# Performance work log

Hardware: AMD Instinct MI355X
Metric: run time of the kernel (lower is better)

## Reference

```python
import jax, jax.numpy as jnp
import numpy as np

D_MODEL = 1024
D_FF = 4096
NUM_EXPERTS = 8
TOP_K = 2


def setup_inputs() -> dict:
    key = jax.random.key(0)
    ks = jax.random.split(key, 8)
    s_in = 1.0 / np.sqrt(D_MODEL)
    s_ff = 1.0 / np.sqrt(D_FF)
    x = jax.random.normal(ks[0], (2, 2048, D_MODEL), dtype=jnp.float32)
    Wg = jax.random.uniform(ks[1], (D_MODEL, NUM_EXPERTS), minval=-s_in, maxval=s_in, dtype=jnp.float32)
    bg = jax.random.uniform(ks[2], (NUM_EXPERTS,), minval=-s_in, maxval=s_in, dtype=jnp.float32)
    W1 = jax.random.uniform(ks[3], (NUM_EXPERTS, D_MODEL, D_FF), minval=-s_in, maxval=s_in, dtype=jnp.float32)
    b1 = jax.random.uniform(ks[4], (NUM_EXPERTS, D_FF), minval=-s_in, maxval=s_in, dtype=jnp.float32)
    W2 = jax.random.uniform(ks[5], (NUM_EXPERTS, D_FF, D_MODEL), minval=-s_ff, maxval=s_ff, dtype=jnp.float32)
    b2 = jax.random.uniform(ks[6], (NUM_EXPERTS, D_MODEL), minval=-s_ff, maxval=s_ff, dtype=jnp.float32)
    return {"x": x, "Wg": Wg, "bg": bg, "W1": W1, "b1": b1, "W2": W2, "b2": b2}


def reference(x, Wg, bg, W1, b1, W2, b2):
    # Gating: softmax over experts, top-k, renormalize
    gate_logits = jnp.einsum('bsd,de->bse', x, Wg) + bg
    gate_probs = jax.nn.softmax(gate_logits, axis=-1)
    topk_probs, topk_idx = jax.lax.top_k(gate_probs, TOP_K)
    topk_probs = topk_probs / jnp.sum(topk_probs, axis=-1, keepdims=True)
    # Per-token combine weights over experts [B,S,E] (top-k indices are unique)
    onehot = jax.nn.one_hot(topk_idx, NUM_EXPERTS, dtype=x.dtype)  # [B,S,K,E]
    weights = jnp.einsum('bske,bsk->bse', onehot, topk_probs)
    # Dense per-expert FFN (exact GELU matches torch nn.GELU default)
    h = jnp.einsum('bsd,edf->bsef', x, W1) + b1  # [B,S,E,Dff]
    h = jax.nn.gelu(h, approximate=False)
    y = jnp.einsum('bsef,efd->bsed', h, W2) + b2  # [B,S,E,D]
    return jnp.einsum('bsed,bse->bsd', y, weights)
```

## Files before the change

kernel.cpp:

```cpp
#include <hip/hip_runtime.h>
#include <hip/hip_bf16.h>
#include <math.h>

#define D_MODEL 1024
#define D_FF    4096
#define NE      8
#define NTOK    4096
#define MAXTOK  4096
#define MAXROWS 9216
#define MAXMT   72

typedef __attribute__((ext_vector_type(8))) short short8;
typedef __attribute__((ext_vector_type(4))) float f32x4;

#define WS_CNT     0
#define WS_OFFA    128
#define WS_TOKIDS  1024
#define WS_TOKW    (WS_TOKIDS + NE*MAXTOK*4)
#define WS_ROWTOK  (WS_TOKW + NE*MAXTOK*4)
#define WS_ROWW    (WS_ROWTOK + MAXROWS*4)
#define WS_XG      524288
#define WS_H       (WS_XG + (size_t)MAXROWS*D_MODEL*2)
#define WS_W1T     (WS_H + (size_t)MAXROWS*D_FF*2)
#define WS_W2T     (WS_W1T + (size_t)NE*D_MODEL*D_FF*2)
#define WS_NEED    (WS_W2T + (size_t)NE*D_MODEL*D_FF*2)

__device__ __forceinline__ ushort f2b(float v) {
    __hip_bfloat16 b = __float2bfloat16(v);
    return *reinterpret_cast<ushort*>(&b);
}

__device__ __forceinline__ float gelu_f(float v) {
    float z = fabsf(v) * 0.70710678118654752f;
    float t = 1.0f / (1.0f + 0.3275911f * z);
    float p = t * (0.254829592f + t * (-0.284496736f + t * (1.421413741f + t * (-1.453152027f + t * 1.061405429f))));
    float er = 1.0f - p * __expf(-z * z);
    float s = (v >= 0.0f) ? er : -er;
    return 0.5f * v * (1.0f + s);
}

__device__ __forceinline__ int xcd_swz(int orig, int nwg) {
    int q = nwg >> 3, r = nwg & 7;
    int xcd = orig & 7, pos = orig >> 3;
    return (xcd < r ? xcd * (q + 1) : r * (q + 1) + (xcd - r) * q) + pos;
}

__global__ __launch_bounds__(256) void gating_kernel(
    const float* __restrict__ x, const float* __restrict__ Wg, const float* __restrict__ bg,
    int* __restrict__ cnt, int* __restrict__ tok_ids, float* __restrict__ tok_w)
{
    __shared__ float s_wg[D_MODEL * NE];
    int tid = threadIdx.x;
    for (int i = tid; i < D_MODEL * NE; i += 256) s_wg[i] = Wg[i];
    __syncthreads();

    int t = blockIdx.x * 256 + tid;
    float acc[NE];
    #pragma unroll
    for (int e = 0; e < NE; ++e) acc[e] = bg[e];
    const float* xr = x + (size_t)t * D_MODEL;
    for (int d = 0; d < D_MODEL; d += 4) {
        float4 xv = *reinterpret_cast<const float4*>(xr + d);
        #pragma unroll
        for (int e = 0; e < NE; ++e) {
            acc[e] += xv.x * s_wg[(d + 0) * NE + e];
            acc[e] += xv.y * s_wg[(d + 1) * NE + e];
            acc[e] += xv.z * s_wg[(d + 2) * NE + e];
            acc[e] += xv.w * s_wg[(d + 3) * NE + e];
        }
    }
    int i0 = 0;
    #pragma unroll
    for (int e = 1; e < NE; ++e) if (acc[e] > acc[i0]) i0 = e;
    int i1 = (i0 == 0) ? 1 : 0;
    #pragma unroll
    for (int e = 0; e < NE; ++e) if (e != i0 && acc[e] > acc[i1]) i1 = e;
    float e1 = __expf(acc[i1] - acc[i0]);
    float inv = 1.0f / (1.0f + e1);
    float w0 = inv, w1 = e1 * inv;

    int p0 = atomicAdd(&cnt[i0], 1);
    tok_ids[i0 * MAXTOK + p0] = t;  tok_w[i0 * MAXTOK + p0] = w0;
    int p1 = atomicAdd(&cnt[i1], 1);
    tok_ids[i1 * MAXTOK + p1] = t;  tok_w[i1 * MAXTOK + p1] = w1;
}

__global__ void scan_kernel(const int* __restrict__ cnt, int* __restrict__ off) {
    if (threadIdx.x == 0) {
        int acc = 0;
        for (int e = 0; e < NE; ++e) { off[e] = acc; acc += ((cnt[e] + 127) & ~127); }
        off[NE] = acc;
    }
}

__global__ __launch_bounds__(256) void gather_kernel(
    const float* __restrict__ x, const int* __restrict__ cnt, const int* __restrict__ off,
    const int* __restrict__ tok_ids, const float* __restrict__ tok_w,
    ushort* __restrict__ Xg, int* __restrict__ rowtok, float* __restrict__ roww)
{
    int e = blockIdx.y;
    int npad = off[e + 1] - off[e];
    int r0 = blockIdx.x * 128;
    if (r0 >= npad) return;
    int n = cnt[e];
    int base = off[e];
    for (int idx = threadIdx.x; idx < 128 * 128; idx += 256) {
        int r = r0 + (idx >> 7);
        int s = idx & 127;
        int R = base + r;
        int tok = -1;
        float4 v0 = {0, 0, 0, 0}, v1 = {0, 0, 0, 0};
        if (r < n) {
            tok = tok_ids[e * MAXTOK + r];
            const float4* src = (const float4*)(x + (size_t)tok * D_MODEL + s * 8);
            v0 = src[0]; v1 = src[1];
        }
        ushort o[8];
        o[0] = f2b(v0.x); o[1] = f2b(v0.y); o[2] = f2b(v0.z); o[3] = f2b(v0.w);
        o[4] = f2b(v1.x); o[5] = f2b(v1.y); o[6] = f2b(v1.z); o[7] = f2b(v1.w);
        int c = s >> 3, sub = s & 7;
        int ds = sub ^ (R & 7);
        *(uint4*)(Xg + (size_t)R * D_MODEL + c * 64 + ds * 8) = *(const uint4*)o;
        if (s == 0) {
            rowtok[R] = tok;
            roww[R] = (tok >= 0) ? tok_w[e * MAXTOK + r] : 0.0f;
        }
    }
}

__global__ __launch_bounds__(256) void wconv_kernel(
    const float* __restrict__ src, ushort* __restrict__ dst, int K, int N)
{
    __shared__ float st[64][65];
    int e = blockIdx.z;
    int n0 = blockIdx.x * 64;
    int k0 = blockIdx.y * 64;
    const float* s = src + (size_t)e * K * N;
    ushort* d = dst + (size_t)e * N * K;
    for (int i = threadIdx.x; i < 4096; i += 256) {
        int kr = i >> 6, nc = i & 63;
        st[kr][nc] = s[(size_t)(k0 + kr) * N + n0 + nc];
    }
    __syncthreads();
    int c = k0 >> 6;
    #pragma unroll
    for (int it = 0; it < 2; ++it) {
        int v = threadIdx.x + it * 256;
        int nl = v >> 3, sub = v & 7;
        ushort o[8];
        #pragma unroll
        for (int j = 0; j < 8; ++j) o[j] = f2b(st[sub * 8 + j][nl]);
        int ds = sub ^ (nl & 7);
        *(uint4*)(d + (size_t)(n0 + nl) * K + c * 64 + ds * 8) = *(const uint4*)o;
    }
}

__global__ __launch_bounds__(256) void gemm1_kernel(
    const ushort* __restrict__ Xg, const ushort* __restrict__ W1T,
    const float* __restrict__ b1, const int* __restrict__ off,
    ushort* __restrict__ H)
{
    __shared__ ushort sA[2][128 * 64];
    __shared__ ushort sB[2][128 * 64];
    int wid = xcd_swz(blockIdx.x, MAXMT * 32);
    int mt = wid >> 5;
    int nt = wid & 31;
    int row0 = mt << 7;
    if (row0 >= off[NE]) return;
    int e = 0;
    #pragma unroll
    for (int i = 1; i < NE; ++i) if (off[i] <= row0) e = i;
    int nb0 = nt << 7;

    int tid = threadIdx.x;
    int lane = tid & 63, wave = tid >> 6;
    int wr = wave >> 1, wc = wave & 1;
    int lrow = tid >> 3, lslot = tid & 7;

    const ushort* Abase = Xg + (size_t)row0 * D_MODEL;
    const ushort* Bbase = W1T + ((size_t)e * D_FF + nb0) * D_MODEL;

    f32x4 acc[4][4];
    #pragma unroll
    for (int m = 0; m < 4; ++m)
        #pragma unroll
        for (int n = 0; n < 4; ++n)
            acc[m][n] = (f32x4){0.f, 0.f, 0.f, 0.f};

    #define STAGE1(buf, kt) { \
        _Pragma("unroll") \
        for (int r = 0; r < 4; ++r) { \
            int row = r * 32 + lrow; \
            const ushort* ga = Abase + (size_t)row * D_MODEL + (kt) * 64 + lslot * 8; \
            const ushort* gb = Bbase + (size_t)row * D_MODEL + (kt) * 64 + lslot * 8; \
            __builtin_amdgcn_global_load_lds((const __attribute__((address_space(1))) void*)ga, \
                (__attribute__((address_space(3))) void*)(sA[buf] + (size_t)(r * 256 + wave * 64) * 8), 16, 0, 0); \
            __builtin_amdgcn_global_load_lds((const __attribute__((address_space(1))) void*)gb, \
                (__attribute__((address_space(3))) void*)(sB[buf] + (size_t)(r * 256 + wave * 64) * 8), 16, 0, 0); \
        } }

    STAGE1(0, 0);
    __syncthreads();
    for (int kt = 0; kt < D_MODEL / 64; ++kt) {
        int cur = kt & 1;
        if (kt + 1 < D_MODEL / 64) STAGE1(cur ^ 1, kt + 1);
        #pragma unroll
        for (int ks = 0; ks < 2; ++ks) {
            short8 a[4], b[4];
            #pragma unroll
            for (int m = 0; m < 4; ++m) {
                int arow = wr * 64 + m * 16 + (lane & 15);
                int aslot = (ks * 4 + (lane >> 4)) ^ (arow & 7);
                a[m] = *(const short8*)(sA[cur] + arow * 64 + aslot * 8);
            }
            #pragma unroll
            for (int n = 0; n < 4; ++n) {
                int brow = wc * 64 + n * 16 + (lane & 15);
                int bslot = (ks * 4 + (lane >> 4)) ^ (brow & 7);
                b[n] = *(const short8*)(sB[cur] + brow * 64 + bslot * 8);
            }
            #pragma unroll
            for (int m = 0; m < 4; ++m)
                #pragma unroll
                for (int n = 0; n < 4; ++n)
                    acc[m][n] = __builtin_amdgcn_mfma_f32_16x16x32_bf16(a[m], b[n], acc[m][n], 0, 0, 0);
        }
        __syncthreads();
    }

    const float* b1e = b1 + (size_t)e * D_FF;
    #pragma unroll
    for (int m = 0; m < 4; ++m) {
        int rbase = wr * 64 + m * 16 + (lane >> 4) * 4;
        #pragma unroll
        for (int n = 0; n < 4; ++n) {
            int col = nb0 + wc * 64 + n * 16 + (lane & 15);
            float bv = b1e[col];
            int cc = col >> 6, sub = (col >> 3) & 7, el = col & 7;
            #pragma unroll
            for (int q = 0; q < 4; ++q) {
                int R = row0 + rbase + q;
                float v = gelu_f(acc[m][n][q] + bv);
                int ds = sub ^ (R & 7);
                H[(size_t)R * D_FF + cc * 64 + ds * 8 + el] = f2b(v);
            }
        }
    }
}

__global__ __launch_bounds__(256) void gemm2_kernel(
    const ushort* __restrict__ H, const ushort* __restrict__ W2T,
    const float* __restrict__ b2, const int* __restrict__ off,
    const int* __restrict__ rowtok, const float* __restrict__ roww,
    float* __restrict__ out)
{
    __shared__ ushort sA[2][128 * 64];
    __shared__ ushort sB[2][128 * 64];
    int wid = xcd_swz(blockIdx.x, MAXMT * 16);
    int mt = wid >> 4;
    int ks2 = (wid >> 3) & 1;
    int nt = wid & 7;
    int row0 = mt << 7;
    if (row0 >= off[NE]) return;
    int e = 0;
    #pragma unroll
    for (int i = 1; i < NE; ++i) if (off[i] <= row0) e = i;
    int nb0 = nt << 7;

    int tid = threadIdx.x;
    int lane = tid & 63, wave = tid >> 6;
    int wr = wave >> 1, wc = wave & 1;
    int lrow = tid >> 3, lslot = tid & 7;

    const ushort* Abase = H + (size_t)row0 * D_FF;
    const ushort* Bbase = W2T + ((size_t)e * D_MODEL + nb0) * D_FF;

    f32x4 acc[4][4];
    #pragma unroll
    for (int m = 0; m < 4; ++m)
        #pragma unroll
        for (int n = 0; n < 4; ++n)
            acc[m][n] = (f32x4){0.f, 0.f, 0.f, 0.f};

    #define STAGE2(buf, kt) { \
        _Pragma("unroll") \
        for (int r = 0; r < 4; ++r) { \
            int row = r * 32 + lrow; \
            const ushort* ga = Abase + (size_t)row * D_FF + (kt) * 64 + lslot * 8; \
            const ushort* gb = Bbase + (size_t)row * D_FF + (kt) * 64 + lslot * 8; \
            __builtin_amdgcn_global_load_lds((const __attribute__((address_space(1))) void*)ga, \
                (__attribute__((address_space(3))) void*)(sA[buf] + (size_t)(r * 256 + wave * 64) * 8), 16, 0, 0); \
            __builtin_amdgcn_global_load_lds((const __attribute__((address_space(1))) void*)gb, \
                (__attribute__((address_space(3))) void*)(sB[buf] + (size_t)(r * 256 + wave * 64) * 8), 16, 0, 0); \
        } }

    int kt0 = ks2 * 32;
    STAGE2(0, kt0);
    __syncthreads();
    for (int i = 0; i < 32; ++i) {
        int cur = i & 1;
        if (i + 1 < 32) STAGE2(cur ^ 1, kt0 + i + 1);
        #pragma unroll
        for (int ks = 0; ks < 2; ++ks) {
            short8 a[4], b[4];
            #pragma unroll
            for (int m = 0; m < 4; ++m) {
                int arow = wr * 64 + m * 16 + (lane & 15);
                int aslot = (ks * 4 + (lane >> 4)) ^ (arow & 7);
                a[m] = *(const short8*)(sA[cur] + arow * 64 + aslot * 8);
            }
            #pragma unroll
            for (int n = 0; n < 4; ++n) {
                int brow = wc * 64 + n * 16 + (lane & 15);
                int bslot = (ks * 4 + (lane >> 4)) ^ (brow & 7);
                b[n] = *(const short8*)(sB[cur] + brow * 64 + bslot * 8);
            }
            #pragma unroll
            for (int m = 0; m < 4; ++m)
                #pragma unroll
                for (int n = 0; n < 4; ++n)
                    acc[m][n] = __builtin_amdgcn_mfma_f32_16x16x32_bf16(a[m], b[n], acc[m][n], 0, 0, 0);
        }
        __syncthreads();
    }

    const float* b2e = b2 + (size_t)e * D_MODEL;
    #pragma unroll
    for (int m = 0; m < 4; ++m) {
        int rbase = wr * 64 + m * 16 + (lane >> 4) * 4;
        #pragma unroll
        for (int n = 0; n < 4; ++n) {
            int col = nb0 + wc * 64 + n * 16 + (lane & 15);
            float bv = (ks2 == 0) ? b2e[col] : 0.0f;
            #pragma unroll
            for (int q = 0; q < 4; ++q) {
                int R = row0 + rbase + q;
                int tok = rowtok[R];
                if (tok >= 0) {
                    float y = roww[R] * (acc[m][n][q] + bv);
                    atomicAdd(out + (size_t)tok * D_MODEL + col, y);
                }
            }
        }
    }
}

#define TM      32
#define FFC     128
#define KSTEP   64

__global__ __launch_bounds__(512) void ffn_kernel(
    const float* __restrict__ x,
    const float* __restrict__ W1, const float* __restrict__ b1,
    const float* __restrict__ W2, const float* __restrict__ b2,
    const int* __restrict__ cnt, const int* __restrict__ tok_ids, const float* __restrict__ tok_w,
    float* __restrict__ out)
{
    int e = blockIdx.y;
    int n = cnt[e];
    int t0 = blockIdx.x * TM;
    if (t0 >= n) return;
    int tid = threadIdx.x;

    __shared__ int   s_tok[TM];
    __shared__ float s_w[TM];
    __shared__ float s_x[TM][KSTEP];
    __shared__ float s_w1[KSTEP][FFC];
    __shared__ float s_h[TM][FFC];

    if (tid < TM) {
        int idx = t0 + tid;
        s_tok[tid] = (idx < n) ? tok_ids[e * MAXTOK + idx] : -1;
        s_w[tid]   = (idx < n) ? tok_w[e * MAXTOK + idx] : 0.0f;
    }
    __syncthreads();

    float acc[TM][2];
    #pragma unroll
    for (int i = 0; i < TM; ++i) { acc[i][0] = 0.0f; acc[i][1] = 0.0f; }

    const float* W1e = W1 + (size_t)e * D_MODEL * D_FF;
    const float* W2e = W2 + (size_t)e * D_FF * D_MODEL;
    const float* b1e = b1 + (size_t)e * D_FF;

    int ffl = (tid & 63) * 2;
    int g   = tid >> 6;

    int fb0 = blockIdx.z * (D_FF / 2);
    for (int fb = fb0; fb < fb0 + D_FF / 2; fb += FFC) {
        float bv0 = b1e[fb + ffl], bv1 = b1e[fb + ffl + 1];
        float hacc[4][2];
        #pragma unroll
        for (int j = 0; j < 4; ++j) { hacc[j][0] = bv0; hacc[j][1] = bv1; }

        for (int kb = 0; kb < D_MODEL; kb += KSTEP) {
            #pragma unroll
            for (int r = 0; r < 4; ++r) {
                int i = tid + 512 * r;
                int row = i >> 6, col = i & 63;
                int tok = s_tok[row];
                s_x[row][col] = (tok >= 0) ? x[(size_t)tok * D_MODEL + kb + col] : 0.0f;
            }
            #pragma unroll
            for (int r = 0; r < 16; ++r) {
                int i = tid + 512 * r;
                int row = i >> 7, col = i & 127;
                s_w1[row][col] = W1e[(size_t)(kb + row) * D_FF + fb + col];
            }
            __syncthreads();
            #pragma unroll 8
            for (int kk = 0; kk < KSTEP; ++kk) {
                float2 wv = *reinterpret_cast<const float2*>(&s_w1[kk][ffl]);
                #pragma unroll
                for (int j = 0; j < 4; ++j) {
                    float xv = s_x[g * 4 + j][kk];
                    hacc[j][0] += xv * wv.x;
                    hacc[j][1] += xv * wv.y;
                }
            }
            __syncthreads();
        }
        #pragma unroll
        for (int j = 0; j < 4; ++j) {
            #pragma unroll
            for (int p = 0; p < 2; ++p) {
                float v = hacc[j][p];
                v = 0.5f * v * (1.0f + erff(v * 0.70710678118654752f));
                s_h[g * 4 + j][ffl + p] = v;
            }
        }
        __syncthreads();
        for (int ff = 0; ff < FFC; ++ff) {
            const float* w2row = W2e + (size_t)(fb + ff) * D_MODEL;
            float wc0 = w2row[tid], wc1 = w2row[tid + 512];
            #pragma unroll
            for (int tt = 0; tt < TM; ++tt) {
                float hv = s_h[tt][ff];
                acc[tt][0] += hv * wc0;
                acc[tt][1] += hv * wc1;
            }
        }
        __syncthreads();
    }

    float bc0 = b2[(size_t)e * D_MODEL + tid];
    float bc1 = b2[(size_t)e * D_MODEL + tid + 512];
    if (blockIdx.z != 0) { bc0 = 0.0f; bc1 = 0.0f; }
    #pragma unroll
    for (int tt = 0; tt < TM; ++tt) {
        int tok = s_tok[tt];
        if (tok >= 0) {
            float w = s_w[tt];
            atomicAdd(&out[(size_t)tok * D_MODEL + tid],       w * (acc[tt][0] + bc0));
            atomicAdd(&out[(size_t)tok * D_MODEL + tid + 512], w * (acc[tt][1] + bc1));
        }
    }
}

extern "C" void kernel_launch(void* const* d_in, const int* in_sizes, int n_in,
                              void* d_out, int out_size, void* d_ws, size_t ws_size,
                              hipStream_t stream) {
    const float* x  = (const float*)d_in[0];
    const float* Wg = (const float*)d_in[1];
    const float* bg = (const float*)d_in[2];
    const float* W1 = (const float*)d_in[3];
    const float* b1 = (const float*)d_in[4];
    const float* W2 = (const float*)d_in[5];
    const float* b2 = (const float*)d_in[6];
    float* out = (float*)d_out;

    char* ws = (char*)d_ws;
    int*    cnt     = (int*)(ws + WS_CNT);
    int*    offp    = (int*)(ws + WS_OFFA);
    int*    tok_ids = (int*)(ws + WS_TOKIDS);
    float*  tok_w   = (float*)(ws + WS_TOKW);

    hipMemsetAsync(cnt, 0, NE * sizeof(int), stream);
    hipMemsetAsync(out, 0, (size_t)out_size * sizeof(float), stream);

    gating_kernel<<<NTOK / 256, 256, 0, stream>>>(x, Wg, bg, cnt, tok_ids, tok_w);

    if (ws_size >= WS_NEED) {
        int*    rowtok = (int*)(ws + WS_ROWTOK);
        float*  roww   = (float*)(ws + WS_ROWW);
        ushort* Xg     = (ushort*)(ws + WS_XG);
        ushort* Hb     = (ushort*)(ws + WS_H);
        ushort* W1T    = (ushort*)(ws + WS_W1T);
        ushort* W2T    = (ushort*)(ws + WS_W2T);

        scan_kernel<<<1, 64, 0, stream>>>(cnt, offp);
        wconv_kernel<<<dim3(D_FF / 64, D_MODEL / 64, NE), 256, 0, stream>>>(W1, W1T, D_MODEL, D_FF);
        wconv_kernel<<<dim3(D_MODEL / 64, D_FF / 64, NE), 256, 0, stream>>>(W2, W2T, D_FF, D_MODEL);
        gather_kernel<<<dim3(32, NE), 256, 0, stream>>>(x, cnt, offp, tok_ids, tok_w, Xg, rowtok, roww);
        gemm1_kernel<<<MAXMT * 32, 256, 0, stream>>>(Xg, W1T, b1, offp, Hb);
        gemm2_kernel<<<MAXMT * 16, 256, 0, stream>>>(Hb, W2T, b2, offp, rowtok, roww, out);
    } else {
        dim3 grid(MAXTOK / TM, NE, 2);
        ffn_kernel<<<grid, 512, 0, stream>>>(x, W1, b1, W2, b2, cnt, tok_ids, tok_w, out);
    }
}
```

Measured before the change: 570.3 us.

## Use 256x256 GEMM tiles with split-K partial buffers and deterministic combine kernel

Adds a new path that pads expert segments to 256 rows and runs both expert GEMMs with 256x256 tiles on 512-thread blocks, raising arithmetic intensity per LDS load. GEMM2 now writes split-K partial outputs into a workspace buffer (aliasing the dead W1T region) instead of atomically accumulating into the output. A per-token combine kernel sums the partials and applies gate weights, which removes the output memset and the atomics. The cost is more padding rows, an extra kernel with extra fp32 traffic, and a larger workspace requirement, with the old 128-tile path kept as a fallback.

After: 482.1 us. -15.5%, faster.

```diff
diff --git a/kernel.cpp b/kernel.cpp
--- a/kernel.cpp
+++ b/kernel.cpp
@@ -7,8 +7,11 @@
 #define NE      8
 #define NTOK    4096
 #define MAXTOK  4096
-#define MAXROWS 9216
-#define MAXMT   72
+
+#define MAXROWS 10240
+#define MAXMT   40
+#define MAXROWSB 9216
+#define MAXMTB   72
 
 typedef __attribute__((ext_vector_type(8))) short short8;
 typedef __attribute__((ext_vector_type(4))) float f32x4;
@@ -19,11 +22,19 @@
 #define WS_TOKW    (WS_TOKIDS + NE*MAXTOK*4)
 #define WS_ROWTOK  (WS_TOKW + NE*MAXTOK*4)
 #define WS_ROWW    (WS_ROWTOK + MAXROWS*4)
-#define WS_XG      524288
-#define WS_H       (WS_XG + (size_t)MAXROWS*D_MODEL*2)
-#define WS_W1T     (WS_H + (size_t)MAXROWS*D_FF*2)
-#define WS_W2T     (WS_W1T + (size_t)NE*D_MODEL*D_FF*2)
-#define WS_NEED    (WS_W2T + (size_t)NE*D_MODEL*D_FF*2)
+#define WS_TOKEXP  (WS_ROWW + MAXROWS*4)
+
+#define WS_H       524288
+#define WS_W1T     (WS_H   + (size_t)MAXROWS*D_FF*2)
+#define WS_XG      (WS_W1T + (size_t)NE*D_MODEL*D_FF*2)
+#define WS_W2T     (WS_XG  + (size_t)MAXROWS*D_MODEL*2)
+#define WS_NEED_A  (WS_W2T + (size_t)NE*D_MODEL*D_FF*2)
+
+#define WSB_XG     524288
+#define WSB_H      (WSB_XG  + (size_t)MAXROWSB*D_MODEL*2)
+#define WSB_W1T    (WSB_H   + (size_t)MAXROWSB*D_FF*2)
+#define WSB_W2T    (WSB_W1T + (size_t)NE*D_MODEL*D_FF*2)
+#define WS_NEED_B  (WSB_W2T + (size_t)NE*D_MODEL*D_FF*2)
 
 __device__ __forceinline__ ushort f2b(float v) {
     __hip_bfloat16 b = __float2bfloat16(v);
@@ -47,7 +58,8 @@
 
 __global__ __launch_bounds__(256) void gating_kernel(
     const float* __restrict__ x, const float* __restrict__ Wg, const float* __restrict__ bg,
-    int* __restrict__ cnt, int* __restrict__ tok_ids, float* __restrict__ tok_w)
+    int* __restrict__ cnt, int* __restrict__ tok_ids, float* __restrict__ tok_w,
+    int* __restrict__ tokexp)
 {
     __shared__ float s_wg[D_MODEL * NE];
     int tid = threadIdx.x;
@@ -81,11 +93,20 @@
 
     int p0 = atomicAdd(&cnt[i0], 1);
     tok_ids[i0 * MAXTOK + p0] = t;  tok_w[i0 * MAXTOK + p0] = w0;
+    tokexp[t * 2 + 0] = i0 * MAXTOK + p0;
     int p1 = atomicAdd(&cnt[i1], 1);
     tok_ids[i1 * MAXTOK + p1] = t;  tok_w[i1 * MAXTOK + p1] = w1;
-}
-
-__global__ void scan_kernel(const int* __restrict__ cnt, int* __restrict__ off) {
+    tokexp[t * 2 + 1] = i1 * MAXTOK + p1;
+}
+
+__global__ void scan256_kernel(const int* __restrict__ cnt, int* __restrict__ off) {
+    if (threadIdx.x == 0) {
+        int acc = 0;
+        for (int e = 0; e < NE; ++e) { off[e] = acc; acc += ((cnt[e] + 255) & ~255); }
+        off[NE] = acc;
+    }
+}
+__global__ void scan128_kernel(const int* __restrict__ cnt, int* __restrict__ off) {
     if (threadIdx.x == 0) {
         int acc = 0;
         for (int e = 0; e < NE; ++e) { off[e] = acc; acc += ((cnt[e] + 127) & ~127); }
@@ -155,14 +176,224 @@
     }
 }
 
-__global__ __launch_bounds__(256) void gemm1_kernel(
+
+__global__ __launch_bounds__(512, 2) void gemm1_256(
     const ushort* __restrict__ Xg, const ushort* __restrict__ W1T,
     const float* __restrict__ b1, const int* __restrict__ off,
     ushort* __restrict__ H)
 {
+    __shared__ ushort smem[65536];
+    int wid = xcd_swz(blockIdx.x, MAXMT * 16);
+    int mt = wid >> 4, nt = wid & 15;
+    int row0 = mt << 8;
+    if (row0 >= off[NE]) return;
+    int e = 0;
+    #pragma unroll
+    for (int i = 1; i < NE; ++i) if (off[i] <= row0) e = i;
+    int nb0 = nt << 8;
+    int tid = threadIdx.x;
+    int lane = tid & 63, wave = tid >> 6;
+    int wr = wave >> 2, wc = wave & 3;
+
+    const ushort* Abase = Xg + (size_t)row0 * D_MODEL;
+    const ushort* Bbase = W1T + ((size_t)e * D_FF + nb0) * D_MODEL;
+
+    f32x4 acc[8][4];
+    #pragma unroll
+    for (int m = 0; m < 8; ++m)
+        #pragma unroll
+        for (int n = 0; n < 4; ++n)
+            acc[m][n] = (f32x4){0.f, 0.f, 0.f, 0.f};
+
+    #define STAGE1(buf, kt) { \
+        _Pragma("unroll") \
+        for (int r = 0; r < 4; ++r) { \
+            int flat = r * 512 + tid; int row_ = flat >> 3, sl = flat & 7; \
+            __builtin_amdgcn_global_load_lds((const __attribute__((address_space(1))) void*)(Abase + (size_t)row_ * D_MODEL + (kt) * 64 + sl * 8), \
+                (__attribute__((address_space(3))) void*)(smem + (buf) * 16384 + flat * 8), 16, 0, 0); \
+            __builtin_amdgcn_global_load_lds((const __attribute__((address_space(1))) void*)(Bbase + (size_t)row_ * D_MODEL + (kt) * 64 + sl * 8), \
+                (__attribute__((address_space(3))) void*)(smem + 32768 + (buf) * 16384 + flat * 8), 16, 0, 0); \
+        } }
+
+    STAGE1(0, 0);
+    __syncthreads();
+    for (int kt = 0; kt < 16; ++kt) {
+        int cur = kt & 1;
+        if (kt + 1 < 16) STAGE1(cur ^ 1, kt + 1);
+        const ushort* sAc = smem + cur * 16384;
+        const ushort* sBc = smem + 32768 + cur * 16384;
+        #pragma unroll
+        for (int ks = 0; ks < 2; ++ks) {
+            int j = ks * 4 + (lane >> 4);
+            short8 b[4];
+            #pragma unroll
+            for (int n = 0; n < 4; ++n) {
+                int brow = wc * 64 + n * 16 + (lane & 15);
+                b[n] = *(const short8*)(sBc + brow * 64 + (j ^ (brow & 7)) * 8);
+            }
+            #pragma unroll
+            for (int m = 0; m < 8; ++m) {
+                int arow = wr * 128 + m * 16 + (lane & 15);
+                short8 a = *(const short8*)(sAc + arow * 64 + (j ^ (arow & 7)) * 8);
+                #pragma unroll
+                for (int n = 0; n < 4; ++n)
+                    acc[m][n] = __builtin_amdgcn_mfma_f32_16x16x32_bf16(a, b[n], acc[m][n], 0, 0, 0);
+            }
+        }
+        __syncthreads();
+    }
+
+    const float* b1e = b1 + (size_t)e * D_FF + nb0;
+    #pragma unroll
+    for (int n = 0; n < 4; ++n) {
+        int col = wc * 64 + n * 16 + (lane & 15);
+        float bv = b1e[col];
+        int gl = col >> 3, el = col & 7;
+        #pragma unroll
+        for (int m = 0; m < 8; ++m) {
+            int rbase = wr * 128 + m * 16 + (lane >> 4) * 4;
+            #pragma unroll
+            for (int q = 0; q < 4; ++q) {
+                int row = rbase + q;
+                float v = gelu_f(acc[m][n][q] + bv);
+                int g = (gl & ~7) | ((gl ^ row) & 7);
+                smem[row * 256 + g * 8 + el] = f2b(v);
+            }
+        }
+    }
+    __syncthreads();
+    #pragma unroll
+    for (int it = 0; it < 16; ++it) {
+        int flat = it * 512 + tid;
+        int row = flat >> 5, g = flat & 31;
+        *(uint4*)(H + (size_t)(row0 + row) * D_FF + nb0 + g * 8) = *(const uint4*)(smem + flat * 8);
+    }
+}
+
+__global__ __launch_bounds__(512, 2) void gemm2_256(
+    const ushort* __restrict__ H, const ushort* __restrict__ W2T,
+    const float* __restrict__ b2, const int* __restrict__ off,
+    float* __restrict__ Y, int nks)
+{
+    __shared__ ushort smem[65536];
+    int per = 4 * nks;
+    int wid = xcd_swz(blockIdx.x, MAXMT * per);
+    int mt = wid / per;
+    int rrem = wid - mt * per;
+    int nt = rrem & 3, ks = rrem >> 2;
+    int row0 = mt << 8;
+    if (row0 >= off[NE]) return;
+    int e = 0;
+    #pragma unroll
+    for (int i = 1; i < NE; ++i) if (off[i] <= row0) e = i;
+    int nb0 = nt << 8;
+    int tid = threadIdx.x;
+    int lane = tid & 63, wave = tid >> 6;
+    int wr = wave >> 2, wc = wave & 3;
+    int KTS = 64 / nks;
+    int kt0 = ks * KTS;
+
+    const ushort* Abase = H + (size_t)row0 * D_FF;
+    const ushort* Bbase = W2T + ((size_t)e * D_MODEL + nb0) * D_FF;
+
+    f32x4 acc[8][4];
+    #pragma unroll
+    for (int m = 0; m < 8; ++m)
+        #pragma unroll
+        for (int n = 0; n < 4; ++n)
+            acc[m][n] = (f32x4){0.f, 0.f, 0.f, 0.f};
+
+    #define STAGE2(buf, kt) { \
+        _Pragma("unroll") \
+        for (int r = 0; r < 4; ++r) { \
+            int flat = r * 512 + tid; int row_ = flat >> 3, sl = flat & 7; \
+            __builtin_amdgcn_global_load_lds((const __attribute__((address_space(1))) void*)(Abase + (size_t)row_ * D_FF + (kt) * 64 + sl * 8), \
+                (__attribute__((address_space(3))) void*)(smem + (buf) * 16384 + flat * 8), 16, 0, 0); \
+            __builtin_amdgcn_global_load_lds((const __attribute__((address_space(1))) void*)(Bbase + (size_t)row_ * D_FF + (kt) * 64 + sl * 8), \
+                (__attribute__((address_space(3))) void*)(smem + 32768 + (buf) * 16384 + flat * 8), 16, 0, 0); \
+        } }
+
+    STAGE2(0, kt0);
+    __syncthreads();
+    for (int i = 0; i < KTS; ++i) {
+        int cur = i & 1;
+        if (i + 1 < KTS) STAGE2(cur ^ 1, kt0 + i + 1);
+        const ushort* sAc = smem + cur * 16384;
+        const ushort* sBc = smem + 32768 + cur * 16384;
+        #pragma unroll
+        for (int ksu = 0; ksu < 2; ++ksu) {
+            int j = ksu * 4 + (lane >> 4);
+            short8 b[4];
+            #pragma unroll
+            for (int n = 0; n < 4; ++n) {
+                int brow = wc * 64 + n * 16 + (lane & 15);
+                b[n] = *(const short8*)(sBc + brow * 64 + (j ^ (brow & 7)) * 8);
+            }
+            #pragma unroll
+            for (int m = 0; m < 8; ++m) {
+                int arow = wr * 128 + m * 16 + (lane & 15);
+                short8 a = *(const short8*)(sAc + arow * 64 + (j ^ (arow & 7)) * 8);
+                #pragma unroll
+                for (int n = 0; n < 4; ++n)
+                    acc[m][n] = __builtin_amdgcn_mfma_f32_16x16x32_bf16(a, b[n], acc[m][n], 0, 0, 0);
+            }
+        }
+        __syncthreads();
+    }
+
+    float* Yb = Y + (size_t)ks * MAXROWS * D_MODEL;
+    const float* b2e = b2 + (size_t)e * D_MODEL + nb0;
+    #pragma unroll
+    for (int n = 0; n < 4; ++n) {
+        int col = wc * 64 + n * 16 + (lane & 15);
+        float bv = (ks == 0) ? b2e[col] : 0.0f;
+        #pragma unroll
+        for (int m = 0; m < 8; ++m) {
+            int rbase = wr * 128 + m * 16 + (lane >> 4) * 4;
+            #pragma unroll
+            for (int q = 0; q < 4; ++q)
+                Yb[(size_t)(row0 + rbase + q) * D_MODEL + nb0 + col] = acc[m][n][q] + bv;
+        }
+    }
+}
+
+__global__ __launch_bounds__(256) void combine_kernel(
+    const float* __restrict__ Y, const int* __restrict__ off,
+    const int* __restrict__ tokexp, const float* __restrict__ tok_w,
+    float* __restrict__ out, int nks)
+{
+    int t = blockIdx.x;
+    int pos0 = tokexp[2 * t], pos1 = tokexp[2 * t + 1];
+    int e0 = pos0 >> 12, p0 = pos0 & (MAXTOK - 1);
+    int e1 = pos1 >> 12, p1 = pos1 & (MAXTOK - 1);
+    size_t R0 = off[e0] + p0, R1 = off[e1] + p1;
+    float w0 = tok_w[pos0], w1 = tok_w[pos1];
+    int c = threadIdx.x * 4;
+    float y0x = 0, y0y = 0, y0z = 0, y0w = 0;
+    float y1x = 0, y1y = 0, y1z = 0, y1w = 0;
+    for (int s = 0; s < nks; ++s) {
+        const float* Ys = Y + (size_t)s * MAXROWS * D_MODEL;
+        float4 a = *(const float4*)(Ys + R0 * D_MODEL + c);
+        float4 b = *(const float4*)(Ys + R1 * D_MODEL + c);
+        y0x += a.x; y0y += a.y; y0z += a.z; y0w += a.w;
+        y1x += b.x; y1y += b.y; y1z += b.z; y1w += b.w;
+    }
+    float4 o;
+    o.x = w0 * y0x + w1 * y1x;
+    o.y = w0 * y0y + w1 * y1y;
+    o.z = w0 * y0z + w1 * y1z;
+    o.w = w0 * y0w + w1 * y1w;
+    *(float4*)(out + (size_t)t * D_MODEL + c) = o;
+}
+
+__global__ __launch_bounds__(256) void gemm1_128(
+    const ushort* __restrict__ Xg, const ushort* __restrict__ W1T,
+    const float* __restrict__ b1, const int* __restrict__ off,
+    ushort* __restrict__ H)
+{
     __shared__ ushort sA[2][128 * 64];
     __shared__ ushort sB[2][128 * 64];
-    int wid = xcd_swz(blockIdx.x, MAXMT * 32);
+    int wid = xcd_swz(blockIdx.x, MAXMTB * 32);
     int mt = wid >> 5;
     int nt = wid & 31;
     int row0 = mt << 7;
@@ -171,7 +402,6 @@
     #pragma unroll
     for (int i = 1; i < NE; ++i) if (off[i] <= row0) e = i;
     int nb0 = nt << 7;
-
     int tid = threadIdx.x;
     int lane = tid & 63, wave = tid >> 6;
     int wr = wave >> 1, wc = wave & 1;
@@ -187,7 +417,7 @@
         for (int n = 0; n < 4; ++n)
             acc[m][n] = (f32x4){0.f, 0.f, 0.f, 0.f};
 
-    #define STAGE1(buf, kt) { \
+    #define STAGE1B(buf, kt) { \
         _Pragma("unroll") \
         for (int r = 0; r < 4; ++r) { \
             int row = r * 32 + lrow; \
@@ -199,11 +429,11 @@
                 (__attribute__((address_space(3))) void*)(sB[buf] + (size_t)(r * 256 + wave * 64) * 8), 16, 0, 0); \
         } }
 
-    STAGE1(0, 0);
+    STAGE1B(0, 0);
     __syncthreads();
     for (int kt = 0; kt < D_MODEL / 64; ++kt) {
         int cur = kt & 1;
-        if (kt + 1 < D_MODEL / 64) STAGE1(cur ^ 1, kt + 1);
+        if (kt + 1 < D_MODEL / 64) STAGE1B(cur ^ 1, kt + 1);
         #pragma unroll
         for (int ks = 0; ks < 2; ++ks) {
             short8 a[4], b[4];
@@ -248,7 +478,7 @@
     }
 }
 
-__global__ __launch_bounds__(256) void gemm2_kernel(
+__global__ __launch_bounds__(256) void gemm2_128(
     const ushort* __restrict__ H, const ushort* __restrict__ W2T,
     const float* __restrict__ b2, const int* __restrict__ off,
     const int* __restrict__ rowtok, const float* __restrict__ roww,
@@ -256,7 +486,7 @@
 {
     __shared__ ushort sA[2][128 * 64];
     __shared__ ushort sB[2][128 * 64];
-    int wid = xcd_swz(blockIdx.x, MAXMT * 16);
+    int wid = xcd_swz(blockIdx.x, MAXMTB * 16);
     int mt = wid >> 4;
     int ks2 = (wid >> 3) & 1;
     int nt = wid & 7;
@@ -266,7 +496,6 @@
     #pragma unroll
     for (int i = 1; i < NE; ++i) if (off[i] <= row0) e = i;
     int nb0 = nt << 7;
-
     int tid = threadIdx.x;
     int lane = tid & 63, wave = tid >> 6;
     int wr = wave >> 1, wc = wave & 1;
@@ -282,7 +511,7 @@
         for (int n = 0; n < 4; ++n)
             acc[m][n] = (f32x4){0.f, 0.f, 0.f, 0.f};
 
-    #define STAGE2(buf, kt) { \
+    #define STAGE2B(buf, kt) { \
         _Pragma("unroll") \
         for (int r = 0; r < 4; ++r) { \
             int row = r * 32 + lrow; \
@@ -295,11 +524,11 @@
         } }
 
     int kt0 = ks2 * 32;
-    STAGE2(0, kt0);
+    STAGE2B(0, kt0);
     __syncthreads();
     for (int i = 0; i < 32; ++i) {
         int cur = i & 1;
-        if (i + 1 < 32) STAGE2(cur ^ 1, kt0 + i + 1);
+        if (i + 1 < 32) STAGE2B(cur ^ 1, kt0 + i + 1);
         #pragma unroll
         for (int ks = 0; ks < 2; ++ks) {
             short8 a[4], b[4];
@@ -474,27 +703,43 @@
     int*    offp    = (int*)(ws + WS_OFFA);
     int*    tok_ids = (int*)(ws + WS_TOKIDS);
     float*  tok_w   = (float*)(ws + WS_TOKW);
+    int*    rowtok  = (int*)(ws + WS_ROWTOK);
+    float*  roww    = (float*)(ws + WS_ROWW);
+    int*    tokexp  = (int*)(ws + WS_TOKEXP);
 
     hipMemsetAsync(cnt, 0, NE * sizeof(int), stream);
-    hipMemsetAsync(out, 0, (size_t)out_size * sizeof(float), stream);
-
-    gating_kernel<<<NTOK / 256, 256, 0, stream>>>(x, Wg, bg, cnt, tok_ids, tok_w);
-
-    if (ws_size >= WS_NEED) {
-        int*    rowtok = (int*)(ws + WS_ROWTOK);
-        float*  roww   = (float*)(ws + WS_ROWW);
-        ushort* Xg     = (ushort*)(ws + WS_XG);
-        ushort* Hb     = (ushort*)(ws + WS_H);
-        ushort* W1T    = (ushort*)(ws + WS_W1T);
-        ushort* W2T    = (ushort*)(ws + WS_W2T);
-
-        scan_kernel<<<1, 64, 0, stream>>>(cnt, offp);
+    gating_kernel<<<NTOK / 256, 256, 0, stream>>>(x, Wg, bg, cnt, tok_ids, tok_w, tokexp);
+
+    if (ws_size >= WS_NEED_A) {
+        ushort* Hb  = (ushort*)(ws + WS_H);
+        ushort* W1T = (ushort*)(ws + WS_W1T);
+        ushort* Xg  = (ushort*)(ws + WS_XG);
+        ushort* W2T = (ushort*)(ws + WS_W2T);
+        float*  Y   = (float*)(ws + WS_W1T);
+        const int nks = 2;
+
+        scan256_kernel<<<1, 64, 0, stream>>>(cnt, offp);
         wconv_kernel<<<dim3(D_FF / 64, D_MODEL / 64, NE), 256, 0, stream>>>(W1, W1T, D_MODEL, D_FF);
         wconv_kernel<<<dim3(D_MODEL / 64, D_FF / 64, NE), 256, 0, stream>>>(W2, W2T, D_FF, D_MODEL);
         gather_kernel<<<dim3(32, NE), 256, 0, stream>>>(x, cnt, offp, tok_ids, tok_w, Xg, rowtok, roww);
-        gemm1_kernel<<<MAXMT * 32, 256, 0, stream>>>(Xg, W1T, b1, offp, Hb);
-        gemm2_kernel<<<MAXMT * 16, 256, 0, stream>>>(Hb, W2T, b2, offp, rowtok, roww, out);
+        gemm1_256<<<MAXMT * 16, 512, 0, stream>>>(Xg, W1T, b1, offp, Hb);
+        gemm2_256<<<MAXMT * 4 * nks, 512, 0, stream>>>(Hb, W2T, b2, offp, Y, nks);
+        combine_kernel<<<NTOK, 256, 0, stream>>>(Y, offp, tokexp, tok_w, out, nks);
+    } else if (ws_size >= WS_NEED_B) {
+        ushort* Xg  = (ushort*)(ws + WSB_XG);
+        ushort* Hb  = (ushort*)(ws + WSB_H);
+        ushort* W1T = (ushort*)(ws + WSB_W1T);
+        ushort* W2T = (ushort*)(ws + WSB_W2T);
+
+        hipMemsetAsync(out, 0, (size_t)out_size * sizeof(float), stream);
+        scan128_kernel<<<1, 64, 0, stream>>>(cnt, offp);
+        wconv_kernel<<<dim3(D_FF / 64, D_MODEL / 64, NE), 256, 0, stream>>>(W1, W1T, D_MODEL, D_FF);
+        wconv_kernel<<<dim3(D_MODEL / 64, D_FF / 64, NE), 256, 0, stream>>>(W2, W2T, D_FF, D_MODEL);
+        gather_kernel<<<dim3(32, NE), 256, 0, stream>>>(x, cnt, offp, tok_ids, tok_w, Xg, rowtok, roww);
+        gemm1_128<<<MAXMTB * 32, 256, 0, stream>>>(Xg, W1T, b1, offp, Hb);
+        gemm2_128<<<MAXMTB * 16, 256, 0, stream>>>(Hb, W2T, b2, offp, rowtok, roww, out);
     } else {
+        hipMemsetAsync(out, 0, (size_t)out_size * sizeof(float), stream);
         dim3 grid(MAXTOK / TM, NE, 2);
         ffn_kernel<<<grid, 512, 0, stream>>>(x, W1, b1, W2, b2, cnt, tok_ids, tok_w, out);
     }
```

## Use 256x256 GEMM tiles with 512 threads, supertile order, and LDS-staged H stores

Applied to the files above, without the earlier changes.

Both expert GEMMs move from 128x128 tiles with 256 threads to 256x256 tiles with 512 threads, each wave holding an 8x4 MFMA accumulator. Blocks are ordered in 4x4 supertiles for L2 reuse, and per-expert row padding grows to 256. GEMM1 now stages its GELU output through swizzled LDS so H is written with coalesced 16-byte stores. GEMM2 splits K four ways instead of two, which means more float atomics on the output, and the two weight-conversion kernels are merged into one launch. Larger tiles cut the global and LDS traffic per FLOP, but they add padding waste and register pressure and leave fewer blocks to fill the CUs.

Result: slower. 636.5 us (+11.6%).

```diff
diff --git a/kernel.cpp b/kernel.cpp
--- a/kernel.cpp
+++ b/kernel.cpp
@@ -7,8 +7,10 @@
 #define NE      8
 #define NTOK    4096
 #define MAXTOK  4096
-#define MAXROWS 9216
-#define MAXMT   72
+
+#define MAXROWS 10240
+#define MAXMT   40
+#define MSUP    10
 
 typedef __attribute__((ext_vector_type(8))) short short8;
 typedef __attribute__((ext_vector_type(4))) float f32x4;
@@ -19,11 +21,13 @@
 #define WS_TOKW    (WS_TOKIDS + NE*MAXTOK*4)
 #define WS_ROWTOK  (WS_TOKW + NE*MAXTOK*4)
 #define WS_ROWW    (WS_ROWTOK + MAXROWS*4)
-#define WS_XG      524288
-#define WS_H       (WS_XG + (size_t)MAXROWS*D_MODEL*2)
-#define WS_W1T     (WS_H + (size_t)MAXROWS*D_FF*2)
-#define WS_W2T     (WS_W1T + (size_t)NE*D_MODEL*D_FF*2)
-#define WS_NEED    (WS_W2T + (size_t)NE*D_MODEL*D_FF*2)
+#define WS_TOKEXP  (WS_ROWW + MAXROWS*4)
+
+#define WS_H       524288
+#define WS_W1T     (WS_H   + (size_t)MAXROWS*D_FF*2)
+#define WS_XG      (WS_W1T + (size_t)NE*D_MODEL*D_FF*2)
+#define WS_W2T     (WS_XG  + (size_t)MAXROWS*D_MODEL*2)
+#define WS_NEED_A  (WS_W2T + (size_t)NE*D_MODEL*D_FF*2)
 
 __device__ __forceinline__ ushort f2b(float v) {
     __hip_bfloat16 b = __float2bfloat16(v);
@@ -85,10 +89,10 @@
     tok_ids[i1 * MAXTOK + p1] = t;  tok_w[i1 * MAXTOK + p1] = w1;
 }
 
-__global__ void scan_kernel(const int* __restrict__ cnt, int* __restrict__ off) {
+__global__ void scan256_kernel(const int* __restrict__ cnt, int* __restrict__ off) {
     if (threadIdx.x == 0) {
         int acc = 0;
-        for (int e = 0; e < NE; ++e) { off[e] = acc; acc += ((cnt[e] + 127) & ~127); }
+        for (int e = 0; e < NE; ++e) { off[e] = acc; acc += ((cnt[e] + 255) & ~255); }
         off[NE] = acc;
     }
 }
@@ -128,15 +132,19 @@
     }
 }
 
-__global__ __launch_bounds__(256) void wconv_kernel(
-    const float* __restrict__ src, ushort* __restrict__ dst, int K, int N)
+__global__ __launch_bounds__(256) void wconv_all(
+    const float* __restrict__ W1, const float* __restrict__ W2,
+    ushort* __restrict__ W1T, ushort* __restrict__ W2T)
 {
     __shared__ float st[64][65];
-    int e = blockIdx.z;
-    int n0 = blockIdx.x * 64;
-    int k0 = blockIdx.y * 64;
-    const float* s = src + (size_t)e * K * N;
-    ushort* d = dst + (size_t)e * N * K;
+    int z = blockIdx.y;
+    const float* s; ushort* d; int K, N;
+    if (z < 8) { s = W1 + (size_t)z * D_MODEL * D_FF;       d = W1T + (size_t)z * D_MODEL * D_FF; K = D_MODEL; N = D_FF; }
+    else       { s = W2 + (size_t)(z - 8) * D_FF * D_MODEL; d = W2T + (size_t)(z - 8) * D_FF * D_MODEL; K = D_FF; N = D_MODEL; }
+    int nblk = N >> 6;
+    int bx = blockIdx.x;
+    int n0 = (bx % nblk) * 64;
+    int k0 = (bx / nblk) * 64;
     for (int i = threadIdx.x; i < 4096; i += 256) {
         int kr = i >> 6, nc = i & 63;
         st[kr][nc] = s[(size_t)(k0 + kr) * N + n0 + nc];
@@ -150,39 +158,39 @@
         ushort o[8];
         #pragma unroll
         for (int j = 0; j < 8; ++j) o[j] = f2b(st[sub * 8 + j][nl]);
-        int ds = sub ^ (nl & 7);
+        int ds = sub ^ ((n0 + nl) & 7);
         *(uint4*)(d + (size_t)(n0 + nl) * K + c * 64 + ds * 8) = *(const uint4*)o;
     }
 }
 
-__global__ __launch_bounds__(256) void gemm1_kernel(
+
+__global__ __launch_bounds__(512, 2) void gemm1_256(
     const ushort* __restrict__ Xg, const ushort* __restrict__ W1T,
     const float* __restrict__ b1, const int* __restrict__ off,
     ushort* __restrict__ H)
 {
-    __shared__ ushort sA[2][128 * 64];
-    __shared__ ushort sB[2][128 * 64];
-    int wid = xcd_swz(blockIdx.x, MAXMT * 32);
-    int mt = wid >> 5;
-    int nt = wid & 31;
-    int row0 = mt << 7;
+    __shared__ ushort smem[65536];
+    int wid = xcd_swz(blockIdx.x, MSUP * 4 * 16);
+    int S = wid >> 4, t16 = wid & 15;
+    int msup = S >> 2, nsup = S & 3;
+    int mt = msup * 4 + (t16 & 3);
+    int nt = nsup * 4 + (t16 >> 2);
+    int row0 = mt << 8;
     if (row0 >= off[NE]) return;
     int e = 0;
     #pragma unroll
     for (int i = 1; i < NE; ++i) if (off[i] <= row0) e = i;
-    int nb0 = nt << 7;
-
+    int nb0 = nt << 8;
     int tid = threadIdx.x;
     int lane = tid & 63, wave = tid >> 6;
-    int wr = wave >> 1, wc = wave & 1;
-    int lrow = tid >> 3, lslot = tid & 7;
+    int wr = wave >> 2, wc = wave & 3;
 
     const ushort* Abase = Xg + (size_t)row0 * D_MODEL;
     const ushort* Bbase = W1T + ((size_t)e * D_FF + nb0) * D_MODEL;
 
-    f32x4 acc[4][4];
-    #pragma unroll
-    for (int m = 0; m < 4; ++m)
+    f32x4 acc[8][4];
+    #pragma unroll
+    for (int m = 0; m < 8; ++m)
         #pragma unroll
         for (int n = 0; n < 4; ++n)
             acc[m][n] = (f32x4){0.f, 0.f, 0.f, 0.f};
@@ -190,94 +198,97 @@
     #define STAGE1(buf, kt) { \
         _Pragma("unroll") \
         for (int r = 0; r < 4; ++r) { \
-            int row = r * 32 + lrow; \
-            const ushort* ga = Abase + (size_t)row * D_MODEL + (kt) * 64 + lslot * 8; \
-            const ushort* gb = Bbase + (size_t)row * D_MODEL + (kt) * 64 + lslot * 8; \
-            __builtin_amdgcn_global_load_lds((const __attribute__((address_space(1))) void*)ga, \
-                (__attribute__((address_space(3))) void*)(sA[buf] + (size_t)(r * 256 + wave * 64) * 8), 16, 0, 0); \
-            __builtin_amdgcn_global_load_lds((const __attribute__((address_space(1))) void*)gb, \
-                (__attribute__((address_space(3))) void*)(sB[buf] + (size_t)(r * 256 + wave * 64) * 8), 16, 0, 0); \
+            int flat = r * 512 + tid; int row_ = flat >> 3, sl = flat & 7; \
+            __builtin_amdgcn_global_load_lds((const __attribute__((address_space(1))) void*)(Abase + (size_t)row_ * D_MODEL + (kt) * 64 + sl * 8), \
+                (__attribute__((address_space(3))) void*)(smem + (buf) * 16384 + flat * 8), 16, 0, 0); \
+            __builtin_amdgcn_global_load_lds((const __attribute__((address_space(1))) void*)(Bbase + (size_t)row_ * D_MODEL + (kt) * 64 + sl * 8), \
+                (__attribute__((address_space(3))) void*)(smem + 32768 + (buf) * 16384 + flat * 8), 16, 0, 0); \
         } }
 
     STAGE1(0, 0);
     __syncthreads();
-    for (int kt = 0; kt < D_MODEL / 64; ++kt) {
+    for (int kt = 0; kt < 16; ++kt) {
         int cur = kt & 1;
-        if (kt + 1 < D_MODEL / 64) STAGE1(cur ^ 1, kt + 1);
+        if (kt + 1 < 16) STAGE1(cur ^ 1, kt + 1);
+        const ushort* sAc = smem + cur * 16384;
+        const ushort* sBc = smem + 32768 + cur * 16384;
         #pragma unroll
         for (int ks = 0; ks < 2; ++ks) {
-            short8 a[4], b[4];
-            #pragma unroll
-            for (int m = 0; m < 4; ++m) {
-                int arow = wr * 64 + m * 16 + (lane & 15);
-                int aslot = (ks * 4 + (lane >> 4)) ^ (arow & 7);
-                a[m] = *(const short8*)(sA[cur] + arow * 64 + aslot * 8);
-            }
+            int j = ks * 4 + (lane >> 4);
+            short8 b[4];
             #pragma unroll
             for (int n = 0; n < 4; ++n) {
                 int brow = wc * 64 + n * 16 + (lane & 15);
-                int bslot = (ks * 4 + (lane >> 4)) ^ (brow & 7);
-                b[n] = *(const short8*)(sB[cur] + brow * 64 + bslot * 8);
-            }
-            #pragma unroll
-            for (int m = 0; m < 4; ++m)
+                b[n] = *(const short8*)(sBc + brow * 64 + (j ^ (brow & 7)) * 8);
+            }
+            #pragma unroll
+            for (int m = 0; m < 8; ++m) {
+                int arow = wr * 128 + m * 16 + (lane & 15);
+                short8 a = *(const short8*)(sAc + arow * 64 + (j ^ (arow & 7)) * 8);
                 #pragma unroll
                 for (int n = 0; n < 4; ++n)
-                    acc[m][n] = __builtin_amdgcn_mfma_f32_16x16x32_bf16(a[m], b[n], acc[m][n], 0, 0, 0);
+                    acc[m][n] = __builtin_amdgcn_mfma_f32_16x16x32_bf16(a, b[n], acc[m][n], 0, 0, 0);
+            }
         }
         __syncthreads();
     }
 
-    const float* b1e = b1 + (size_t)e * D_FF;
-    #pragma unroll
-    for (int m = 0; m < 4; ++m) {
-        int rbase = wr * 64 + m * 16 + (lane >> 4) * 4;
-        #pragma unroll
-        for (int n = 0; n < 4; ++n) {
-            int col = nb0 + wc * 64 + n * 16 + (lane & 15);
-            float bv = b1e[col];
-            int cc = col >> 6, sub = (col >> 3) & 7, el = col & 7;
+    const float* b1e = b1 + (size_t)e * D_FF + nb0;
+    #pragma unroll
+    for (int n = 0; n < 4; ++n) {
+        int col = wc * 64 + n * 16 + (lane & 15);
+        float bv = b1e[col];
+        int gl = col >> 3, el = col & 7;
+        #pragma unroll
+        for (int m = 0; m < 8; ++m) {
+            int rbase = wr * 128 + m * 16 + (lane >> 4) * 4;
             #pragma unroll
             for (int q = 0; q < 4; ++q) {
-                int R = row0 + rbase + q;
+                int row = rbase + q;
                 float v = gelu_f(acc[m][n][q] + bv);
-                int ds = sub ^ (R & 7);
-                H[(size_t)R * D_FF + cc * 64 + ds * 8 + el] = f2b(v);
-            }
-        }
-    }
-}
-
-__global__ __launch_bounds__(256) void gemm2_kernel(
+                int g = (gl & ~7) | ((gl ^ row) & 7);
+                smem[row * 256 + g * 8 + el] = f2b(v);
+            }
+        }
+    }
+    __syncthreads();
+    #pragma unroll
+    for (int it = 0; it < 16; ++it) {
+        int flat = it * 512 + tid;
+        int row = flat >> 5, g = flat & 31;
+        *(uint4*)(H + (size_t)(row0 + row) * D_FF + nb0 + g * 8) = *(const uint4*)(smem + flat * 8);
+    }
+}
+
+__global__ __launch_bounds__(512, 2) void gemm2_256(
     const ushort* __restrict__ H, const ushort* __restrict__ W2T,
     const float* __restrict__ b2, const int* __restrict__ off,
     const int* __restrict__ rowtok, const float* __restrict__ roww,
     float* __restrict__ out)
 {
-    __shared__ ushort sA[2][128 * 64];
-    __shared__ ushort sB[2][128 * 64];
-    int wid = xcd_swz(blockIdx.x, MAXMT * 16);
-    int mt = wid >> 4;
-    int ks2 = (wid >> 3) & 1;
-    int nt = wid & 7;
-    int row0 = mt << 7;
+    __shared__ ushort smem[65536];
+    int wid = xcd_swz(blockIdx.x, 4 * MSUP * 16);
+    int S = wid >> 4, t16 = wid & 15;
+    int ks = S / MSUP, msup = S - ks * MSUP;
+    int mt = msup * 4 + (t16 >> 2);
+    int nt = t16 & 3;
+    int row0 = mt << 8;
     if (row0 >= off[NE]) return;
     int e = 0;
     #pragma unroll
     for (int i = 1; i < NE; ++i) if (off[i] <= row0) e = i;
-    int nb0 = nt << 7;
-
+    int nb0 = nt << 8;
     int tid = threadIdx.x;
     int lane = tid & 63, wave = tid >> 6;
-    int wr = wave >> 1, wc = wave & 1;
-    int lrow = tid >> 3, lslot = tid & 7;
+    int wr = wave >> 2, wc = wave & 3;
+    int kt0 = ks * 16;
 
     const ushort* Abase = H + (size_t)row0 * D_FF;
     const ushort* Bbase = W2T + ((size_t)e * D_MODEL + nb0) * D_FF;
 
-    f32x4 acc[4][4];
-    #pragma unroll
-    for (int m = 0; m < 4; ++m)
+    f32x4 acc[8][4];
+    #pragma unroll
+    for (int m = 0; m < 8; ++m)
         #pragma unroll
         for (int n = 0; n < 4; ++n)
             acc[m][n] = (f32x4){0.f, 0.f, 0.f, 0.f};
@@ -285,61 +296,57 @@
     #define STAGE2(buf, kt) { \
         _Pragma("unroll") \
         for (int r = 0; r < 4; ++r) { \
-            int row = r * 32 + lrow; \
-            const ushort* ga = Abase + (size_t)row * D_FF + (kt) * 64 + lslot * 8; \
-            const ushort* gb = Bbase + (size_t)row * D_FF + (kt) * 64 + lslot * 8; \
-            __builtin_amdgcn_global_load_lds((const __attribute__((address_space(1))) void*)ga, \
-                (__attribute__((address_space(3))) void*)(sA[buf] + (size_t)(r * 256 + wave * 64) * 8), 16, 0, 0); \
-            __builtin_amdgcn_global_load_lds((const __attribute__((address_space(1))) void*)gb, \
-                (__attribute__((address_space(3))) void*)(sB[buf] + (size_t)(r * 256 + wave * 64) * 8), 16, 0, 0); \
+            int flat = r * 512 + tid; int row_ = flat >> 3, sl = flat & 7; \
+            __builtin_amdgcn_global_load_lds((const __attribute__((address_space(1))) void*)(Abase + (size_t)row_ * D_FF + (kt) * 64 + sl * 8), \
+                (__attribute__((address_space(3))) void*)(smem + (buf) * 16384 + flat * 8), 16, 0, 0); \
+            __builtin_amdgcn_global_load_lds((const __attribute__((address_space(1))) void*)(Bbase + (size_t)row_ * D_FF + (kt) * 64 + sl * 8), \
+                (__attribute__((address_space(3))) void*)(smem + 32768 + (buf) * 16384 + flat * 8), 16, 0, 0); \
         } }
 
-    int kt0 = ks2 * 32;
     STAGE2(0, kt0);
     __syncthreads();
-    for (int i = 0; i < 32; ++i) {
+    for (int i = 0; i < 16; ++i) {
         int cur = i & 1;
-        if (i + 1 < 32) STAGE2(cur ^ 1, kt0 + i + 1);
-        #pragma unroll
-        for (int ks = 0; ks < 2; ++ks) {
-            short8 a[4], b[4];
-            #pragma unroll
-            for (int m = 0; m < 4; ++m) {
-                int arow = wr * 64 + m * 16 + (lane & 15);
-                int aslot = (ks * 4 + (lane >> 4)) ^ (arow & 7);
-                a[m] = *(const short8*)(sA[cur] + arow * 64 + aslot * 8);
-            }
+        if (i + 1 < 16) STAGE2(cur ^ 1, kt0 + i + 1);
+        const ushort* sAc = smem + cur * 16384;
+        const ushort* sBc = smem + 32768 + cur * 16384;
+        #pragma unroll
+        for (int ksu = 0; ksu < 2; ++ksu) {
+            int j = ksu * 4 + (lane >> 4);
+            short8 b[4];
             #pragma unroll
             for (int n = 0; n < 4; ++n) {
                 int brow = wc * 64 + n * 16 + (lane & 15);
-                int bslot = (ks * 4 + (lane >> 4)) ^ (brow & 7);
-                b[n] = *(const short8*)(sB[cur] + brow * 64 + bslot * 8);
-            }
-            #pragma unroll
-            for (int m = 0; m < 4; ++m)
+                b[n] = *(const short8*)(sBc + brow * 64 + (j ^ (brow & 7)) * 8);
+            }
+            #pragma unroll
+            for (int m = 0; m < 8; ++m) {
+                int arow = wr * 128 + m * 16 + (lane & 15);
+                short8 a = *(const short8*)(sAc + arow * 64 + (j ^ (arow & 7)) * 8);
                 #pragma unroll
                 for (int n = 0; n < 4; ++n)
-                    acc[m][n] = __builtin_amdgcn_mfma_f32_16x16x32_bf16(a[m], b[n], acc[m][n], 0, 0, 0);
+                    acc[m][n] = __builtin_amdgcn_mfma_f32_16x16x32_bf16(a, b[n], acc[m][n], 0, 0, 0);
+            }
         }
         __syncthreads();
     }
 
-    const float* b2e = b2 + (size_t)e * D_MODEL;
-    #pragma unroll
-    for (int m = 0; m < 4; ++m) {
-        int rbase = wr * 64 + m * 16 + (lane >> 4) * 4;
-        #pragma unroll
-        for (int n = 0; n < 4; ++n) {
-            int col = nb0 + wc * 64 + n * 16 + (lane & 15);
-            float bv = (ks2 == 0) ? b2e[col] : 0.0f;
-            #pragma unroll
-            for (int q = 0; q < 4; ++q) {
-                int R = row0 + rbase + q;
-                int tok = rowtok[R];
-                if (tok >= 0) {
-                    float y = roww[R] * (acc[m][n][q] + bv);
-                    atomicAdd(out + (size_t)tok * D_MODEL + col, y);
-                }
+    const float* b2e = b2 + (size_t)e * D_MODEL + nb0;
+    #pragma unroll
+    for (int m = 0; m < 8; ++m) {
+        int rbase = wr * 128 + m * 16 + (lane >> 4) * 4;
+        #pragma unroll
+        for (int q = 0; q < 4; ++q) {
+            int R = row0 + rbase + q;
+            int tok = rowtok[R];
+            if (tok < 0) continue;
+            float w = roww[R];
+            float* orow = out + (size_t)tok * D_MODEL + nb0;
+            #pragma unroll
+            for (int n = 0; n < 4; ++n) {
+                int col = wc * 64 + n * 16 + (lane & 15);
+                float bv = (ks == 0) ? b2e[col] : 0.0f;
+                atomicAdd(orow + col, w * (acc[m][n][q] + bv));
             }
         }
     }
@@ -474,26 +481,24 @@
     int*    offp    = (int*)(ws + WS_OFFA);
     int*    tok_ids = (int*)(ws + WS_TOKIDS);
     float*  tok_w   = (float*)(ws + WS_TOKW);
+    int*    rowtok  = (int*)(ws + WS_ROWTOK);
+    float*  roww    = (float*)(ws + WS_ROWW);
 
     hipMemsetAsync(cnt, 0, NE * sizeof(int), stream);
     hipMemsetAsync(out, 0, (size_t)out_size * sizeof(float), stream);
-
     gating_kernel<<<NTOK / 256, 256, 0, stream>>>(x, Wg, bg, cnt, tok_ids, tok_w);
 
-    if (ws_size >= WS_NEED) {
-        int*    rowtok = (int*)(ws + WS_ROWTOK);
-        float*  roww   = (float*)(ws + WS_ROWW);
-        ushort* Xg     = (ushort*)(ws + WS_XG);
-        ushort* Hb     = (ushort*)(ws + WS_H);
-        ushort* W1T    = (ushort*)(ws + WS_W1T);
-        ushort* W2T    = (ushort*)(ws + WS_W2T);
-
-        scan_kernel<<<1, 64, 0, stream>>>(cnt, offp);
-        wconv_kernel<<<dim3(D_FF / 64, D_MODEL / 64, NE), 256, 0, stream>>>(W1, W1T, D_MODEL, D_FF);
-        wconv_kernel<<<dim3(D_MODEL / 64, D_FF / 64, NE), 256, 0, stream>>>(W2, W2T, D_FF, D_MODEL);
+    if (ws_size >= WS_NEED_A) {
+        ushort* Hb  = (ushort*)(ws + WS_H);
+        ushort* W1T = (ushort*)(ws + WS_W1T);
+        ushort* Xg  = (ushort*)(ws + WS_XG);
+        ushort* W2T = (ushort*)(ws + WS_W2T);
+
+        scan256_kernel<<<1, 64, 0, stream>>>(cnt, offp);
+        wconv_all<<<dim3(1024, 16), 256, 0, stream>>>(W1, W2, W1T, W2T);
         gather_kernel<<<dim3(32, NE), 256, 0, stream>>>(x, cnt, offp, tok_ids, tok_w, Xg, rowtok, roww);
-        gemm1_kernel<<<MAXMT * 32, 256, 0, stream>>>(Xg, W1T, b1, offp, Hb);
-        gemm2_kernel<<<MAXMT * 16, 256, 0, stream>>>(Hb, W2T, b2, offp, rowtok, roww, out);
+        gemm1_256<<<MSUP * 4 * 16, 512, 0, stream>>>(Xg, W1T, b1, offp, Hb);
+        gemm2_256<<<4 * MSUP * 16, 512, 0, stream>>>(Hb, W2T, b2, offp, rowtok, roww, out);
     } else {
         dim3 grid(MAXTOK / TM, NE, 2);
         ffn_kernel<<<grid, 512, 0, stream>>>(x, W1, b1, W2, b2, cnt, tok_ids, tok_w, out);
```
